# Kernel tuning notes

Hardware: AMD Instinct MI355X
Metric: run time of the kernel (lower is better)

The kernel has to match this reference:

```python
import jax, jax.numpy as jnp
import numpy as np

D_MODEL = 256; N_LAYERS = 4; INPUT_LEN = 15
D_INNER = 512; D_STATE = 16; D_CONV = 4; DT_RANK = 16
BATCH = 4; SEQ = 2048; EPS = 1e-5

def _ln(x, w, b):
    m = jnp.mean(x, -1, keepdims=True)
    v = jnp.var(x, -1, keepdims=True)
    return (x - m) * jax.lax.rsqrt(v + EPS) * w + b

def _silu(x):
    return x * jax.nn.sigmoid(x)

def _mixer(h, inW, cw, cb, xpW, dtW, dtb, A_log, Dp, opW):
    # h: [B,L,d_model]
    xz = h @ inW.T                      # [B,L,2*D_INNER]
    xh, z = jnp.split(xz, 2, axis=-1)
    # causal depthwise conv1d
    xc = jnp.transpose(xh, (0, 2, 1))   # [B,D,L]
    xc = jax.lax.conv_general_dilated(xc, cw, (1,), [(D_CONV - 1, 0)],
                                      feature_group_count=D_INNER,
                                      dimension_numbers=('NCH', 'OIH', 'NCH'))
    xc = xc + cb[None, :, None]
    xh = _silu(jnp.transpose(xc, (0, 2, 1)))  # [B,L,D]
    dbl = xh @ xpW.T                    # [B,L,DT_RANK+2N]
    dt = dbl[..., :DT_RANK]
    Bm = dbl[..., DT_RANK:DT_RANK + D_STATE]
    C = dbl[..., DT_RANK + D_STATE:]
    dt = jax.nn.softplus(dt @ dtW.T + dtb)    # [B,L,D]
    A = -jnp.exp(A_log)                       # [D,N]
    dA = jnp.exp(dt[..., None] * A)           # [B,L,D,N]
    dBu = dt[..., None] * Bm[:, :, None, :] * xh[..., None]  # [B,L,D,N]
    def step(hst, inp):
        dA_t, dBu_t, C_t = inp
        hst = dA_t * hst + dBu_t
        y = jnp.einsum('bdn,bn->bd', hst, C_t)
        return hst, y
    h0 = jnp.zeros((xh.shape[0], D_INNER, D_STATE), xh.dtype)
    _, ys = jax.lax.scan(step, h0, (jnp.transpose(dA, (1, 0, 2, 3)),
                                    jnp.transpose(dBu, (1, 0, 2, 3)),
                                    jnp.transpose(C, (1, 0, 2))))
    y = jnp.transpose(ys, (1, 0, 2)) + Dp * xh
    y = y * _silu(z)
    return y @ opW.T

def setup_inputs():
    key = jax.random.key(0)
    ks = jax.random.split(key, 8)
    s = 0.02
    return {
        'x_src': jax.random.normal(ks[0], (BATCH, SEQ, INPUT_LEN), jnp.float32),
        'single_eval_pos': 1024,
        'in_W': jax.random.normal(ks[1], (D_MODEL, INPUT_LEN)) * s,
        'norm_w': jnp.ones((N_LAYERS, D_MODEL)),
        'norm_b': jnp.zeros((N_LAYERS, D_MODEL)),
        'inproj_W': jax.random.normal(ks[2], (N_LAYERS, 2 * D_INNER, D_MODEL)) * s,
        'conv_w': jax.random.normal(ks[3], (N_LAYERS, D_INNER, 1, D_CONV)) * 0.2,
        'conv_b': jnp.zeros((N_LAYERS, D_INNER)),
        'xproj_W': jax.random.normal(ks[4], (N_LAYERS, DT_RANK + 2 * D_STATE, D_INNER)) * s,
        'dtproj_W': jax.random.normal(ks[5], (N_LAYERS, D_INNER, DT_RANK)) * 0.1,
        'dtproj_b': jnp.log(jnp.expm1(jnp.full((N_LAYERS, D_INNER), 0.01))),
        'A_log': jnp.log(jnp.broadcast_to(jnp.arange(1, D_STATE + 1, dtype=jnp.float32), (N_LAYERS, D_INNER, D_STATE)) + 0.0),
        'D_param': jnp.ones((N_LAYERS, D_INNER)),
        'outproj_W': jax.random.normal(ks[6], (N_LAYERS, D_MODEL, D_INNER)) * s,
        'out_W': jax.random.normal(ks[7], (1, D_MODEL)) * s,
    }

def reference(x_src, single_eval_pos, in_W, norm_w, norm_b, inproj_W, conv_w, conv_b, xproj_W, dtproj_W, dtproj_b, A_log, D_param, outproj_W, out_W):
    h = x_src @ in_W.T                  # [B,L,d_model]
    res = None
    for i in range(N_LAYERS):
        res = h if res is None else h + res
        hn = _ln(res, norm_w[i], norm_b[i])
        h = _mixer(hn, inproj_W[i], conv_w[i], conv_b[i], xproj_W[i],
                   dtproj_W[i], dtproj_b[i], A_log[i], D_param[i], outproj_W[i])
    # backbone returns hidden_states directly (norm_f defined but not applied)
    return h @ out_W.T                  # [B,L,1]
```

## Files before the change

### kernel.cpp

```cpp
#include <hip/hip_runtime.h>

#define B_   4
#define T_   2048
#define BT_  8192
#define INL  15
#define DM   256
#define DI   512
#define DX   1024
#define DS_  16
#define DR_  16
#define NO_  48
#define NL   4
#define NC_  128
#define LCH  16

typedef short bf16x8 __attribute__((ext_vector_type(8)));
typedef float f32x4  __attribute__((ext_vector_type(4)));

__device__ __forceinline__ float sigmoidf_(float x){
    return __builtin_amdgcn_rcpf(1.f + __expf(-x));
}
__device__ __forceinline__ float softplusf_(float x){
    return fmaxf(x, 0.f) + __logf(1.f + __expf(-fabsf(x)));
}

__device__ __forceinline__ unsigned short f2bf(float x){
    union { float f; unsigned u; } v; v.f = x;
    unsigned r = (v.u + 0x7FFFu + ((v.u >> 16) & 1u)) >> 16;
    return (unsigned short)r;
}
__device__ __forceinline__ float bf2f(unsigned short h){
    union { unsigned u; float f; } v; v.u = ((unsigned)h) << 16;
    return v.f;
}

__device__ __forceinline__ void ld16(const float* __restrict__ p, float* v){
    const float4* q = (const float4*)p;
    float4 x0=q[0],x1=q[1],x2=q[2],x3=q[3];
    v[0]=x0.x; v[1]=x0.y; v[2]=x0.z; v[3]=x0.w;
    v[4]=x1.x; v[5]=x1.y; v[6]=x1.z; v[7]=x1.w;
    v[8]=x2.x; v[9]=x2.y; v[10]=x2.z; v[11]=x2.w;
    v[12]=x3.x; v[13]=x3.y; v[14]=x3.z; v[15]=x3.w;
}
__device__ __forceinline__ void st16(float* __restrict__ p, const float* v){
    float4* q = (float4*)p;
    q[0] = make_float4(v[0],v[1],v[2],v[3]);
    q[1] = make_float4(v[4],v[5],v[6],v[7]);
    q[2] = make_float4(v[8],v[9],v[10],v[11]);
    q[3] = make_float4(v[12],v[13],v[14],v[15]);
}

__global__ void k_cvtW3(const float* __restrict__ W0, unsigned short* __restrict__ h0,
                        unsigned short* __restrict__ l0, int n0,
                        const float* __restrict__ W1, unsigned short* __restrict__ h1,
                        unsigned short* __restrict__ l1, int n1,
                        const float* __restrict__ W2, unsigned short* __restrict__ h2,
                        unsigned short* __restrict__ l2, int n2){
    int g = blockIdx.x*256 + threadIdx.x;
    const float* W; unsigned short *hi, *lo; int idx;
    if(g < n0){ W = W0; hi = h0; lo = l0; idx = g; }
    else if(g < n0+n1){ W = W1; hi = h1; lo = l1; idx = g - n0; }
    else if(g < n0+n1+n2){ W = W2; hi = h2; lo = l2; idx = g - n0 - n1; }
    else return;
    float4 v = ((const float4*)W)[idx];
    ushort4 h, l;
    h.x = f2bf(v.x); l.x = f2bf(v.x - bf2f(h.x));
    h.y = f2bf(v.y); l.y = f2bf(v.y - bf2f(h.y));
    h.z = f2bf(v.z); l.z = f2bf(v.z - bf2f(h.z));
    h.w = f2bf(v.w); l.w = f2bf(v.w - bf2f(h.w));
    ((ushort4*)hi)[idx] = h;
    ((ushort4*)lo)[idx] = l;
}

__global__ void k_inln(const float* __restrict__ x, const float* __restrict__ W,
                       float* __restrict__ res,
                       unsigned short* __restrict__ hnhi, unsigned short* __restrict__ hnlo,
                       const float* __restrict__ w, const float* __restrict__ b){
    int wv = threadIdx.x >> 6, lane = threadIdx.x & 63;
    int bt = blockIdx.x*4 + wv;
    const float* xr = x + bt*INL;
    float xl[INL];
#pragma unroll
    for(int k=0;k<INL;k++) xl[k] = xr[k];
    float4 v;
    float* vv = (float*)&v;
#pragma unroll
    for(int j=0;j<4;j++){
        int m = lane*4 + j;
        const float* wr = W + m*INL;
        float acc = 0.f;
#pragma unroll
        for(int k=0;k<INL;k++) acc += xl[k]*wr[k];
        vv[j] = acc;
    }
    ((float4*)(res + (size_t)bt*DM))[lane] = v;
    float s  = v.x+v.y+v.z+v.w;
    float ss = v.x*v.x+v.y*v.y+v.z*v.z+v.w*v.w;
#pragma unroll
    for(int m=1;m<64;m<<=1){ s += __shfl_xor(s,m); ss += __shfl_xor(ss,m); }
    float mean = s*(1.f/DM);
    float var  = ss*(1.f/DM) - mean*mean;
    float inv  = rsqrtf(var + 1e-5f);
    float4 wt = ((const float4*)w)[lane];
    float4 bs = ((const float4*)b)[lane];
    float4 o;
    o.x = (v.x-mean)*inv*wt.x + bs.x;
    o.y = (v.y-mean)*inv*wt.y + bs.y;
    o.z = (v.z-mean)*inv*wt.z + bs.z;
    o.w = (v.w-mean)*inv*wt.w + bs.w;
    ushort4 hh, ll;
    hh.x = f2bf(o.x); ll.x = f2bf(o.x - bf2f(hh.x));
    hh.y = f2bf(o.y); ll.y = f2bf(o.y - bf2f(hh.y));
    hh.z = f2bf(o.z); ll.z = f2bf(o.z - bf2f(hh.z));
    hh.w = f2bf(o.w); ll.w = f2bf(o.w - bf2f(hh.w));
    ((ushort4*)(hnhi + (size_t)bt*DM))[lane] = hh;
    ((ushort4*)(hnlo + (size_t)bt*DM))[lane] = ll;
}

__global__ void k_resln(const float* __restrict__ h, float* __restrict__ res,
                        unsigned short* __restrict__ hnhi, unsigned short* __restrict__ hnlo,
                        const float* __restrict__ w, const float* __restrict__ b, int addRes){
    int wv = threadIdx.x >> 6, lane = threadIdx.x & 63;
    int bt = blockIdx.x*4 + wv;
    float4 v = ((const float4*)(h + (size_t)bt*DM))[lane];
    if(addRes){
        float4 r = ((const float4*)(res + (size_t)bt*DM))[lane];
        v.x+=r.x; v.y+=r.y; v.z+=r.z; v.w+=r.w;
    }
    ((float4*)(res + (size_t)bt*DM))[lane] = v;
    float s  = v.x+v.y+v.z+v.w;
    float ss = v.x*v.x+v.y*v.y+v.z*v.z+v.w*v.w;
#pragma unroll
    for(int m=1;m<64;m<<=1){ s += __shfl_xor(s,m); ss += __shfl_xor(ss,m); }
    float mean = s*(1.f/DM);
    float var  = ss*(1.f/DM) - mean*mean;
    float inv  = rsqrtf(var + 1e-5f);
    float4 wt = ((const float4*)w)[lane];
    float4 bs = ((const float4*)b)[lane];
    float4 o;
    o.x = (v.x-mean)*inv*wt.x + bs.x;
    o.y = (v.y-mean)*inv*wt.y + bs.y;
    o.z = (v.z-mean)*inv*wt.z + bs.z;
    o.w = (v.w-mean)*inv*wt.w + bs.w;
    ushort4 hh, ll;
    hh.x = f2bf(o.x); ll.x = f2bf(o.x - bf2f(hh.x));
    hh.y = f2bf(o.y); ll.y = f2bf(o.y - bf2f(hh.y));
    hh.z = f2bf(o.z); ll.z = f2bf(o.z - bf2f(hh.z));
    hh.w = f2bf(o.w); ll.w = f2bf(o.w - bf2f(hh.w));
    ((ushort4*)(hnhi + (size_t)bt*DM))[lane] = hh;
    ((ushort4*)(hnlo + (size_t)bt*DM))[lane] = ll;
}

template<int BM,int BN>
__global__ void __launch_bounds__(256) k_gemm_bf3(
    const unsigned short* __restrict__ Ahi, const unsigned short* __restrict__ Alo,
    const unsigned short* __restrict__ Bhi, const unsigned short* __restrict__ Blo,
    float* __restrict__ C, int M, int N, int K)
{
    constexpr int LDP = 40;
    constexpr int WM = BM/2, WN = BN/2;
    constexpr int MI_ = WM/16, NI_ = WN/16;
    __shared__ unsigned short sAh[BM*LDP], sAl[BM*LDP], sBh[BN*LDP], sBl[BN*LDP];
    int tid  = threadIdx.x;
    int wave = tid >> 6, lane = tid & 63;
    int wm0  = (wave >> 1) * WM, wn0 = (wave & 1) * WN;
    int m0   = blockIdx.y * BM, n0 = blockIdx.x * BN;
    int lr   = lane & 15;
    int kq   = (lane >> 4) * 8;
    int quad4 = (lane >> 4) * 4;

    f32x4 acc[MI_][NI_];
#pragma unroll
    for(int i=0;i<MI_;i++)
#pragma unroll
        for(int j=0;j<NI_;j++) acc[i][j] = (f32x4){0.f,0.f,0.f,0.f};

    for(int k0=0;k0<K;k0+=32){
#pragma unroll
        for(int i=tid;i<BM*4;i+=256){
            int r = i>>2, cg = (i&3)*8;
            size_t go = (size_t)(m0+r)*K + k0 + cg;
            *(float4*)(&sAh[r*LDP + cg]) = *(const float4*)(Ahi + go);
            *(float4*)(&sAl[r*LDP + cg]) = *(const float4*)(Alo + go);
        }
#pragma unroll
        for(int i=tid;i<BN*4;i+=256){
            int r = i>>2, cg = (i&3)*8;
            size_t go = (size_t)(n0+r)*K + k0 + cg;
            *(float4*)(&sBh[r*LDP + cg]) = *(const float4*)(Bhi + go);
            *(float4*)(&sBl[r*LDP + cg]) = *(const float4*)(Blo + go);
        }
        __syncthreads();
        bf16x8 ah[MI_], al[MI_], bh[NI_], bl[NI_];
#pragma unroll
        for(int mi=0;mi<MI_;mi++){
            int ro = (wm0 + mi*16 + lr)*LDP + kq;
            ah[mi] = *(const bf16x8*)(&sAh[ro]);
            al[mi] = *(const bf16x8*)(&sAl[ro]);
        }
#pragma unroll
        for(int ni=0;ni<NI_;ni++){
            int ro = (wn0 + ni*16 + lr)*LDP + kq;
            bh[ni] = *(const bf16x8*)(&sBh[ro]);
            bl[ni] = *(const bf16x8*)(&sBl[ro]);
        }
#pragma unroll
        for(int mi=0;mi<MI_;mi++)
#pragma unroll
            for(int ni=0;ni<NI_;ni++){
                acc[mi][ni] = __builtin_amdgcn_mfma_f32_16x16x32_bf16(ah[mi], bh[ni], acc[mi][ni], 0,0,0);
                acc[mi][ni] = __builtin_amdgcn_mfma_f32_16x16x32_bf16(ah[mi], bl[ni], acc[mi][ni], 0,0,0);
                acc[mi][ni] = __builtin_amdgcn_mfma_f32_16x16x32_bf16(al[mi], bh[ni], acc[mi][ni], 0,0,0);
            }
        __syncthreads();
    }
#pragma unroll
    for(int mi=0;mi<MI_;mi++)
#pragma unroll
        for(int ni=0;ni<NI_;ni++){
            int col = n0 + wn0 + ni*16 + lr;
#pragma unroll
            for(int r=0;r<4;r++){
                int row = m0 + wm0 + mi*16 + quad4 + r;
                C[(size_t)row*N + col] = acc[mi][ni][r];
            }
        }
}

template<int BM,int BN>
__global__ void __launch_bounds__(256) k_gemm_pk(
    const unsigned* __restrict__ Apk,
    const unsigned short* __restrict__ Bhi, const unsigned short* __restrict__ Blo,
    float* __restrict__ C, int M, int N, int K)
{
    constexpr int LDP = 40;
    constexpr int WM = BM/2, WN = BN/2;
    constexpr int MI_ = WM/16, NI_ = WN/16;
    __shared__ unsigned short sAh[BM*LDP], sAl[BM*LDP], sBh[BN*LDP], sBl[BN*LDP];
    int tid  = threadIdx.x;
    int wave = tid >> 6, lane = tid & 63;
    int wm0  = (wave >> 1) * WM, wn0 = (wave & 1) * WN;
    int m0   = blockIdx.y * BM, n0 = blockIdx.x * BN;
    int lr   = lane & 15;
    int kq   = (lane >> 4) * 8;
    int quad4 = (lane >> 4) * 4;

    f32x4 acc[MI_][NI_];
#pragma unroll
    for(int i=0;i<MI_;i++)
#pragma unroll
        for(int j=0;j<NI_;j++) acc[i][j] = (f32x4){0.f,0.f,0.f,0.f};

    for(int k0=0;k0<K;k0+=32){
#pragma unroll
        for(int i=tid;i<BM*2;i+=256){
            int r = i>>1, hf = (i&1)*16;
            const uint4* yp = (const uint4*)(Apk + (size_t)(m0+r)*K + k0 + hf);
#pragma unroll
            for(int q=0;q<4;q++){
                uint4 p = yp[q];
                ushort4 H, L;
                H.x=(unsigned short)p.x;  L.x=(unsigned short)(p.x>>16);
                H.y=(unsigned short)p.y;  L.y=(unsigned short)(p.y>>16);
                H.z=(unsigned short)p.z;  L.z=(unsigned short)(p.z>>16);
                H.w=(unsigned short)p.w;  L.w=(unsigned short)(p.w>>16);
                *(ushort4*)(&sAh[r*LDP + hf + q*4]) = H;
                *(ushort4*)(&sAl[r*LDP + hf + q*4]) = L;
            }
        }
#pragma unroll
        for(int i=tid;i<BN*4;i+=256){
            int r = i>>2, cg = (i&3)*8;
            size_t go = (size_t)(n0+r)*K + k0 + cg;
            *(float4*)(&sBh[r*LDP + cg]) = *(const float4*)(Bhi + go);
            *(float4*)(&sBl[r*LDP + cg]) = *(const float4*)(Blo + go);
        }
        __syncthreads();
        bf16x8 ah[MI_], al[MI_], bh[NI_], bl[NI_];
#pragma unroll
        for(int mi=0;mi<MI_;mi++){
            int ro = (wm0 + mi*16 + lr)*LDP + kq;
            ah[mi] = *(const bf16x8*)(&sAh[ro]);
            al[mi] = *(const bf16x8*)(&sAl[ro]);
        }
#pragma unroll
        for(int ni=0;ni<NI_;ni++){
            int ro = (wn0 + ni*16 + lr)*LDP + kq;
            bh[ni] = *(const bf16x8*)(&sBh[ro]);
            bl[ni] = *(const bf16x8*)(&sBl[ro]);
        }
#pragma unroll
        for(int mi=0;mi<MI_;mi++)
#pragma unroll
            for(int ni=0;ni<NI_;ni++){
                acc[mi][ni] = __builtin_amdgcn_mfma_f32_16x16x32_bf16(ah[mi], bh[ni], acc[mi][ni], 0,0,0);
                acc[mi][ni] = __builtin_amdgcn_mfma_f32_16x16x32_bf16(ah[mi], bl[ni], acc[mi][ni], 0,0,0);
                acc[mi][ni] = __builtin_amdgcn_mfma_f32_16x16x32_bf16(al[mi], bh[ni], acc[mi][ni], 0,0,0);
            }
        __syncthreads();
    }
#pragma unroll
    for(int mi=0;mi<MI_;mi++)
#pragma unroll
        for(int ni=0;ni<NI_;ni++){
            int col = n0 + wn0 + ni*16 + lr;
#pragma unroll
            for(int r=0;r<4;r++){
                int row = m0 + wm0 + mi*16 + quad4 + r;
                C[(size_t)row*N + col] = acc[mi][ni][r];
            }
        }
}

__global__ void __launch_bounds__(512) k_convxp2(
    const float* __restrict__ xz, const float* __restrict__ cw, const float* __restrict__ cb,
    const unsigned short* __restrict__ Bhi, const unsigned short* __restrict__ Blo,
    float* __restrict__ xh, float* __restrict__ dbl)
{
    __shared__ unsigned short sAh[16*520], sAl[16*520];
    __shared__ float sP[6][16][20];

    int tid = threadIdx.x;
    int wave = tid >> 6, lane = tid & 63;
    int lr = lane & 15, kq = (lane>>4)*8, quad4 = (lane>>4)*4;
    int m0 = blockIdx.x * LCH;
    int d  = tid;
    int nt = wave >> 1, kh = wave & 1;

    float xv[19];
    {
        int rbase = m0 - 3;
        bool mask0 = ((m0 & (T_-1)) == 0);
#pragma unroll
        for(int j=0;j<19;j++)
            xv[j] = (mask0 && j<3) ? 0.f : xz[(size_t)(rbase+j)*DX + d];
    }
    bf16x8 pbh[8], pbl[8];
    if(wave < 6){
        const unsigned short* bhp = Bhi + (size_t)(nt*16 + lr)*DI + kh*256 + kq;
        const unsigned short* blp = Blo + (size_t)(nt*16 + lr)*DI + kh*256 + kq;
#pragma unroll
        for(int ks=0;ks<8;ks++){
            pbh[ks] = *(const bf16x8*)(bhp + ks*32);
            pbl[ks] = *(const bf16x8*)(blp + ks*32);
        }
    }
    float4 w4 = *(const float4*)(cw + d*4);
    float bias = cb[d];
#pragma unroll
    for(int t=0;t<16;t++){
        float a = bias + w4.x*xv[t] + w4.y*xv[t+1] + w4.z*xv[t+2] + w4.w*xv[t+3];
        float v = a * sigmoidf_(a);
        xh[(size_t)(m0+t)*DI + d] = v;
        unsigned short hh = f2bf(v);
        sAh[t*520 + d] = hh;
        sAl[t*520 + d] = f2bf(v - bf2f(hh));
    }
    __syncthreads();

    if(wave < 6){
        f32x4 acc = {0.f,0.f,0.f,0.f};
#pragma unroll
        for(int ks=0;ks<8;ks++){
            int ao = lr*520 + kh*256 + ks*32 + kq;
            bf16x8 ah = *(const bf16x8*)(&sAh[ao]);
            bf16x8 al = *(const bf16x8*)(&sAl[ao]);
            acc = __builtin_amdgcn_mfma_f32_16x16x32_bf16(ah, pbh[ks], acc, 0,0,0);
            acc = __builtin_amdgcn_mfma_f32_16x16x32_bf16(ah, pbl[ks], acc, 0,0,0);
            acc = __builtin_amdgcn_mfma_f32_16x16x32_bf16(al, pbh[ks], acc, 0,0,0);
        }
#pragma unroll
        for(int r=0;r<4;r++) sP[wave][quad4+r][lr] = acc[r];
    }
    __syncthreads();

    for(int i=tid;i<768;i+=512){
        int t = i/48, n = i - t*48;
        int nt2 = n >> 4, nn = n & 15;
        float v = sP[nt2*2][t][nn] + sP[nt2*2+1][t][nn];
        dbl[(size_t)(m0+t)*48 + n] = v;
    }
}

__global__ void __launch_bounds__(256) k_scan1(
    const float* __restrict__ dbl, const float* __restrict__ xh,
    const float* __restrict__ dtW, const float* __restrict__ dtbias,
    const float* __restrict__ A_log, float* __restrict__ S, float* __restrict__ sdt)
{
    int d = blockIdx.x*256 + threadIdx.x;
    int c = blockIdx.y, b = blockIdx.z;
    float a_[16]; ld16(A_log + (size_t)d*16, a_);
#pragma unroll
    for(int n=0;n<16;n++) a_[n] = -__expf(a_[n]);
    float wr_[16]; ld16(dtW + (size_t)d*16, wr_);
    float bsv = dtbias[d];
    float st_[16];
#pragma unroll
    for(int n=0;n<16;n++) st_[n] = 0.f;
    float sd = 0.f;
    int base = b*T_ + c*LCH;
#pragma unroll 4
    for(int t=0;t<LCH;t++){
        int bt = base + t;
        float dl[16]; ld16(dbl + (size_t)bt*48, dl);
        float bv[16]; ld16(dbl + (size_t)bt*48 + 16, bv);
        float pre = bsv;
#pragma unroll
        for(int r=0;r<16;r++) pre += dl[r]*wr_[r];
        float dtv = softplusf_(pre);
        float xhv = xh[(size_t)bt*DI + d];
        float dx = dtv*xhv;
        sd += dtv;
#pragma unroll
        for(int n=0;n<16;n++) st_[n] = __expf(dtv*a_[n])*st_[n] + dx*bv[n];
    }
    st16(S + (((size_t)b*NC_ + c)*DI + d)*16, st_);
    sdt[((size_t)b*NC_ + c)*DI + d] = sd;
}

__global__ void k_scan2(const float* __restrict__ S, const float* __restrict__ sdt,
                        const float* __restrict__ A_log, float* __restrict__ Hinit){
    int g = blockIdx.x*256 + threadIdx.x;
    int b = g >> 13;
    int dn = g & 8191;
    int d = dn >> 4;
    float a = -__expf(A_log[dn]);
    float H = 0.f;
    for(int c=0;c<NC_;c++){
        size_t o = ((size_t)(b*NC_ + c))*8192 + dn;
        Hinit[o] = H;
        float sd = sdt[(size_t)(b*NC_ + c)*DI + d];
        H = __expf(sd*a)*H + S[o];
    }
}

__global__ void __launch_bounds__(256) k_scan3(
    const float* __restrict__ dbl, const float* __restrict__ xh, const float* __restrict__ xz,
    const float* __restrict__ A_log, const float* __restrict__ Dpar,
    const float* __restrict__ dtW, const float* __restrict__ dtbias,
    const float* __restrict__ Hinit, unsigned* __restrict__ Y)
{
    __shared__ float sbc[16*52];
    int tid = threadIdx.x;
    int c = blockIdx.y, b = blockIdx.z;
    int m0 = b*T_ + c*LCH;
    if(tid < 192){
        int t = tid/12, s = tid - t*12;
        *(float4*)(&sbc[t*52 + s*4]) = *(const float4*)(dbl + (size_t)(m0+t)*48 + s*4);
    }
    __syncthreads();
    int d = blockIdx.x*256 + tid;
    float a_[16]; ld16(A_log + (size_t)d*16, a_);
#pragma unroll
    for(int n=0;n<16;n++) a_[n] = -__expf(a_[n]);
    float wr_[16]; ld16(dtW + (size_t)d*16, wr_);
    float bsv = dtbias[d];
    float st_[16]; ld16(Hinit + (((size_t)b*NC_ + c)*DI + d)*16, st_);
    float Dp = Dpar[d];
#pragma unroll 2
    for(int t=0;t<LCH;t++){
        int bt = m0 + t;
        float dl[16]; ld16(&sbc[t*52], dl);
        float bv[16]; ld16(&sbc[t*52 + 16], bv);
        float cv[16]; ld16(&sbc[t*52 + 32], cv);
        float pre = bsv;
#pragma unroll
        for(int r=0;r<16;r++) pre += dl[r]*wr_[r];
        float dtv = softplusf_(pre);
        float xhv = xh[(size_t)bt*DI + d];
        float dx = dtv*xhv;
        float y = 0.f;
#pragma unroll
        for(int n=0;n<16;n++){
            st_[n] = __expf(dtv*a_[n])*st_[n] + dx*bv[n];
            y += st_[n]*cv[n];
        }
        float zv = xz[(size_t)bt*DX + DI + d];
        y += Dp*xhv;
        y = y * zv * sigmoidf_(zv);
        unsigned short hh = f2bf(y);
        unsigned short ll = f2bf(y - bf2f(hh));
        Y[(size_t)bt*DI + d] = (unsigned)hh | ((unsigned)ll << 16);
    }
}

__global__ void k_outw(const float* __restrict__ h, const float* __restrict__ ow,
                       float* __restrict__ out){
    int wv = threadIdx.x >> 6, lane = threadIdx.x & 63;
    int bt = blockIdx.x*4 + wv;
    float4 v = ((const float4*)(h + (size_t)bt*DM))[lane];
    float4 w = ((const float4*)ow)[lane];
    float s = v.x*w.x + v.y*w.y + v.z*w.z + v.w*w.w;
#pragma unroll
    for(int m=1;m<64;m<<=1) s += __shfl_xor(s,m);
    if(lane==0) out[bt] = s;
}

extern "C" void kernel_launch(void* const* d_in, const int* in_sizes, int n_in,
                              void* d_out, int out_size, void* d_ws, size_t ws_size,
                              hipStream_t stream){
    const float* x_src    = (const float*)d_in[0];
    const float* in_W     = (const float*)d_in[2];
    const float* norm_w   = (const float*)d_in[3];
    const float* norm_b   = (const float*)d_in[4];
    const float* inproj_W = (const float*)d_in[5];
    const float* conv_w   = (const float*)d_in[6];
    const float* conv_b   = (const float*)d_in[7];
    const float* xproj_W  = (const float*)d_in[8];
    const float* dtproj_W = (const float*)d_in[9];
    const float* dtproj_b = (const float*)d_in[10];
    const float* A_log    = (const float*)d_in[11];
    const float* D_param  = (const float*)d_in[12];
    const float* outproj_W= (const float*)d_in[13];
    const float* out_W    = (const float*)d_in[14];

    float* ws  = (float*)d_ws;
    float* h    = ws;
    float* res  = h    + (size_t)BT_*DM;
    float* xz   = res  + (size_t)BT_*DM;
    float* xh   = xz   + (size_t)BT_*DX;
    float* dbl  = xh   + (size_t)BT_*DI;
    float* sdtb = dbl  + (size_t)BT_*48;
    float* Sbuf = sdtb + (size_t)B_*NC_*DI;
    float* Hbuf = Sbuf + (size_t)B_*NC_*DI*DS_;
    unsigned short* us = (unsigned short*)(Hbuf + (size_t)B_*NC_*DI*DS_);
    unsigned short* WhiIn  = us;
    unsigned short* WloIn  = WhiIn  + (size_t)NL*DX*DM;
    unsigned short* WhiOut = WloIn  + (size_t)NL*DX*DM;
    unsigned short* WloOut = WhiOut + (size_t)NL*DM*DI;
    unsigned short* WhiXp  = WloOut + (size_t)NL*DM*DI;
    unsigned short* WloXp  = WhiXp  + (size_t)NL*NO_*DI;
    unsigned short* hnhi   = WloXp  + (size_t)NL*NO_*DI;
    unsigned short* hnlo   = hnhi   + (size_t)BT_*DM;
    unsigned*       ybuf   = (unsigned*)(hnlo + (size_t)BT_*DM);

    int n0 = NL*DX*DM/4, n1 = NL*DM*DI/4, n2 = NL*NO_*DI/4;
    k_cvtW3<<<(n0+n1+n2 + 255)/256, 256, 0, stream>>>(
        inproj_W,  WhiIn,  WloIn,  n0,
        outproj_W, WhiOut, WloOut, n1,
        xproj_W,   WhiXp,  WloXp,  n2);
    k_inln<<<BT_/4, 256, 0, stream>>>(x_src, in_W, res, hnhi, hnlo, norm_w, norm_b);
    for(int i=0;i<NL;i++){
        if(i > 0)
            k_resln<<<BT_/4, 256, 0, stream>>>(h, res, hnhi, hnlo, norm_w + i*DM, norm_b + i*DM, 1);
        k_gemm_bf3<128,128><<<dim3(DX/128, BT_/128), 256, 0, stream>>>(
            hnhi, hnlo, WhiIn + (size_t)i*DX*DM, WloIn + (size_t)i*DX*DM, xz, BT_, DX, DM);
        k_convxp2<<<BT_/LCH, 512, 0, stream>>>(xz, conv_w + i*DI*4, conv_b + i*DI,
            WhiXp + (size_t)i*NO_*DI, WloXp + (size_t)i*NO_*DI, xh, dbl);
        k_scan1<<<dim3(2, NC_, B_), 256, 0, stream>>>(dbl, xh,
            dtproj_W + (size_t)i*DI*DR_, dtproj_b + i*DI,
            A_log + (size_t)i*DI*DS_, Sbuf, sdtb);
        k_scan2<<<B_*DI*DS_/256, 256, 0, stream>>>(Sbuf, sdtb, A_log + (size_t)i*DI*DS_, Hbuf);
        k_scan3<<<dim3(2, NC_, B_), 256, 0, stream>>>(dbl, xh, xz,
            A_log + (size_t)i*DI*DS_, D_param + i*DI,
            dtproj_W + (size_t)i*DI*DR_, dtproj_b + i*DI, Hbuf, ybuf);
        k_gemm_pk<128,64><<<dim3(DM/64, BT_/128), 256, 0, stream>>>(
            ybuf, WhiOut + (size_t)i*DM*DI, WloOut + (size_t)i*DM*DI, h, BT_, DM, DI);
    }
    k_outw<<<BT_/4, 256, 0, stream>>>(h, out_W, (float*)d_out);
}
```

Baseline: 579.1 us.

## Fuse chunk-scan pass one into conv/x-proj kernel and batch loads in scan kernels

Merges the first chunked-scan pass into the conv+x_proj kernel. Each block reuses the xh and dbl values it just computed from shared memory instead of reloading them from global memory in a separate launch. The cross-chunk scan now loads eight chunks of S and sdt at once to hide latency, and scan3 prefetches xh and z for all 16 timesteps into registers. The costs are more shared memory per block (about 36KB more), higher register pressure under a launch_bounds(512,4) hint, and one fewer kernel launch per layer.

```diff
diff --git a/kernel.cpp b/kernel.cpp
--- a/kernel.cpp
+++ b/kernel.cpp
@@ -312,13 +312,18 @@
         }
 }
 
-__global__ void __launch_bounds__(512) k_convxp2(
+__global__ void __launch_bounds__(512,4) k_convxp2(
     const float* __restrict__ xz, const float* __restrict__ cw, const float* __restrict__ cb,
     const unsigned short* __restrict__ Bhi, const unsigned short* __restrict__ Blo,
-    float* __restrict__ xh, float* __restrict__ dbl)
+    const float* __restrict__ dtW, const float* __restrict__ dtbias,
+    const float* __restrict__ A_log,
+    float* __restrict__ xh, float* __restrict__ dbl,
+    float* __restrict__ S, float* __restrict__ sdt)
 {
     __shared__ unsigned short sAh[16*520], sAl[16*520];
     __shared__ float sP[6][16][20];
+    __shared__ float sXh[16*512];
+    __shared__ float sD[16*52];
 
     int tid = threadIdx.x;
     int wave = tid >> 6, lane = tid & 63;
@@ -352,10 +357,16 @@
         float a = bias + w4.x*xv[t] + w4.y*xv[t+1] + w4.z*xv[t+2] + w4.w*xv[t+3];
         float v = a * sigmoidf_(a);
         xh[(size_t)(m0+t)*DI + d] = v;
+        sXh[t*512 + d] = v;
         unsigned short hh = f2bf(v);
         sAh[t*520 + d] = hh;
         sAl[t*520 + d] = f2bf(v - bf2f(hh));
     }
+    float a_[16]; ld16(A_log + (size_t)d*16, a_);
+#pragma unroll
+    for(int n=0;n<16;n++) a_[n] = -__expf(a_[n]);
+    float wr_[16]; ld16(dtW + (size_t)d*16, wr_);
+    float bsv = dtbias[d];
     __syncthreads();
 
     if(wave < 6){
@@ -379,36 +390,25 @@
         int nt2 = n >> 4, nn = n & 15;
         float v = sP[nt2*2][t][nn] + sP[nt2*2+1][t][nn];
         dbl[(size_t)(m0+t)*48 + n] = v;
-    }
-}
-
-__global__ void __launch_bounds__(256) k_scan1(
-    const float* __restrict__ dbl, const float* __restrict__ xh,
-    const float* __restrict__ dtW, const float* __restrict__ dtbias,
-    const float* __restrict__ A_log, float* __restrict__ S, float* __restrict__ sdt)
-{
-    int d = blockIdx.x*256 + threadIdx.x;
-    int c = blockIdx.y, b = blockIdx.z;
-    float a_[16]; ld16(A_log + (size_t)d*16, a_);
-#pragma unroll
-    for(int n=0;n<16;n++) a_[n] = -__expf(a_[n]);
-    float wr_[16]; ld16(dtW + (size_t)d*16, wr_);
-    float bsv = dtbias[d];
+        sD[t*52 + n] = v;
+    }
+    __syncthreads();
+
+    int b = m0 >> 11;
+    int c = (m0 & (T_-1)) >> 4;
     float st_[16];
 #pragma unroll
     for(int n=0;n<16;n++) st_[n] = 0.f;
     float sd = 0.f;
-    int base = b*T_ + c*LCH;
 #pragma unroll 4
-    for(int t=0;t<LCH;t++){
-        int bt = base + t;
-        float dl[16]; ld16(dbl + (size_t)bt*48, dl);
-        float bv[16]; ld16(dbl + (size_t)bt*48 + 16, bv);
+    for(int t=0;t<16;t++){
+        float dl[16]; ld16(&sD[t*52], dl);
+        float bv[16]; ld16(&sD[t*52 + 16], bv);
         float pre = bsv;
 #pragma unroll
         for(int r=0;r<16;r++) pre += dl[r]*wr_[r];
         float dtv = softplusf_(pre);
-        float xhv = xh[(size_t)bt*DI + d];
+        float xhv = sXh[t*512 + d];
         float dx = dtv*xhv;
         sd += dtv;
 #pragma unroll
@@ -426,11 +426,19 @@
     int d = dn >> 4;
     float a = -__expf(A_log[dn]);
     float H = 0.f;
-    for(int c=0;c<NC_;c++){
-        size_t o = ((size_t)(b*NC_ + c))*8192 + dn;
-        Hinit[o] = H;
-        float sd = sdt[(size_t)(b*NC_ + c)*DI + d];
-        H = __expf(sd*a)*H + S[o];
+    for(int c0=0;c0<NC_;c0+=8){
+        float sv[8], gv[8];
+#pragma unroll
+        for(int j=0;j<8;j++){
+            sv[j] = S[((size_t)(b*NC_ + c0 + j))*8192 + dn];
+            gv[j] = sdt[(size_t)(b*NC_ + c0 + j)*DI + d];
+        }
+#pragma unroll
+        for(int j=0;j<8;j++){
+            size_t o = ((size_t)(b*NC_ + c0 + j))*8192 + dn;
+            Hinit[o] = H;
+            H = __expf(gv[j]*a)*H + sv[j];
+        }
     }
 }
 
@@ -450,6 +458,12 @@
     }
     __syncthreads();
     int d = blockIdx.x*256 + tid;
+    float xhp[16], zvp[16];
+#pragma unroll
+    for(int t=0;t<16;t++){
+        xhp[t] = xh[(size_t)(m0+t)*DI + d];
+        zvp[t] = xz[(size_t)(m0+t)*DX + DI + d];
+    }
     float a_[16]; ld16(A_log + (size_t)d*16, a_);
 #pragma unroll
     for(int n=0;n<16;n++) a_[n] = -__expf(a_[n]);
@@ -467,7 +481,7 @@
 #pragma unroll
         for(int r=0;r<16;r++) pre += dl[r]*wr_[r];
         float dtv = softplusf_(pre);
-        float xhv = xh[(size_t)bt*DI + d];
+        float xhv = xhp[t];
         float dx = dtv*xhv;
         float y = 0.f;
 #pragma unroll
@@ -475,7 +489,7 @@
             st_[n] = __expf(dtv*a_[n])*st_[n] + dx*bv[n];
             y += st_[n]*cv[n];
         }
-        float zv = xz[(size_t)bt*DX + DI + d];
+        float zv = zvp[t];
         y += Dp*xhv;
         y = y * zv * sigmoidf_(zv);
         unsigned short hh = f2bf(y);
@@ -546,10 +560,9 @@
         k_gemm_bf3<128,128><<<dim3(DX/128, BT_/128), 256, 0, stream>>>(
             hnhi, hnlo, WhiIn + (size_t)i*DX*DM, WloIn + (size_t)i*DX*DM, xz, BT_, DX, DM);
         k_convxp2<<<BT_/LCH, 512, 0, stream>>>(xz, conv_w + i*DI*4, conv_b + i*DI,
-            WhiXp + (size_t)i*NO_*DI, WloXp + (size_t)i*NO_*DI, xh, dbl);
-        k_scan1<<<dim3(2, NC_, B_), 256, 0, stream>>>(dbl, xh,
+            WhiXp + (size_t)i*NO_*DI, WloXp + (size_t)i*NO_*DI,
             dtproj_W + (size_t)i*DI*DR_, dtproj_b + i*DI,
-            A_log + (size_t)i*DI*DS_, Sbuf, sdtb);
+            A_log + (size_t)i*DI*DS_, xh, dbl, Sbuf, sdtb);
         k_scan2<<<B_*DI*DS_/256, 256, 0, stream>>>(Sbuf, sdtb, A_log + (size_t)i*DI*DS_, Hbuf);
         k_scan3<<<dim3(2, NC_, B_), 256, 0, stream>>>(dbl, xh, xz,
             A_log + (size_t)i*DI*DS_, D_param + i*DI,
```

New measurement: 596.6 us. 1.03x slower.
